# Kernel optimization log

Measured on AMD Instinct MI355X. Metric: run time of the kernel, lower is better.

## Reference

```python
import jax, jax.numpy as jnp
import numpy as np

B, S, D, H = 2, 2048, 1024, 16
DK = D // H


def setup_inputs() -> dict:
    key = jax.random.key(0)
    ks = jax.random.split(key, 12)
    scale = 1.0 / np.sqrt(D)
    inp = {
        "Q": jax.random.normal(ks[0], (B, S, D), jnp.float32),
        "K": jax.random.normal(ks[1], (B, S, D), jnp.float32),
        "V": jax.random.normal(ks[2], (B, S, D), jnp.float32),
        # causal mask, broadcastable to [B, H, S, S]; 0 -> masked
        "Mask": jnp.tril(jnp.ones((S, S), jnp.int32))[None, None],
        "Wq": jax.random.normal(ks[3], (D, D), jnp.float32) * scale,
        "bq": jnp.zeros((D,), jnp.float32),
        "Wk": jax.random.normal(ks[4], (D, D), jnp.float32) * scale,
        "bk": jnp.zeros((D,), jnp.float32),
        "Wv": jax.random.normal(ks[5], (D, D), jnp.float32) * scale,
        "bv": jnp.zeros((D,), jnp.float32),
        "Wo": jax.random.normal(ks[6], (D, D), jnp.float32) * scale,
        "bo": jnp.zeros((D,), jnp.float32),
    }
    return inp


def _heads(x):
    # [B, S, D] -> [B, H, S, DK]
    return x.reshape(B, S, H, DK).transpose(0, 2, 1, 3)


def reference(Q, K, V, Mask, Wq, bq, Wk, bk, Wv, bv, Wo, bo):
    q = _heads(Q @ Wq.T + bq)
    k = _heads(K @ Wk.T + bk)
    v = _heads(V @ Wv.T + bv)
    # NOTE: original module does NOT scale by 1/sqrt(d_k)
    logits = jnp.einsum("bhqd,bhkd->bhqk", q, k)
    logits = jnp.where(Mask == 0, jnp.float32(-1e9), logits)
    attn = jax.nn.softmax(logits, axis=-1)  # dropout p=0.0 -> identity
    ctx = jnp.einsum("bhqk,bhkd->bhqd", attn, v)
    ctx = ctx.transpose(0, 2, 1, 3).reshape(B, S, D)
    return ctx @ Wo.T + bo
```

## Files before the change

kernel.cpp:

```cpp
#include <hip/hip_runtime.h>
#include <hip/hip_bf16.h>

#define B_  2
#define S_  2048
#define D_  1024
#define H_  16
#define DK_ 64
#define M_  (B_ * S_)

typedef __bf16 bf16;
typedef __bf16 bf16x8 __attribute__((ext_vector_type(8)));
typedef __bf16 bf16x4 __attribute__((ext_vector_type(4)));
typedef float  f32x4  __attribute__((ext_vector_type(4)));

#define MFMA16(a, b, c) __builtin_amdgcn_mfma_f32_16x16x32_bf16((a), (b), (c), 0, 0, 0)

__device__ __forceinline__ void gl2lds16(const bf16* g, bf16* l) {
    __builtin_amdgcn_global_load_lds((const __attribute__((address_space(1))) void*)g,
                                     (__attribute__((address_space(3))) void*)l, 16, 0, 0);
}

struct CastArgs { const float* src[7]; bf16* dst[7]; };

__global__ __launch_bounds__(256) void cast_all(CastArgs a) {
    int i = blockIdx.x * 256 + threadIdx.x;
    int seg, off;
    if (i < 3145728) { seg = i >> 20; off = i & 1048575; }
    else { int j = i - 3145728; seg = 3 + (j >> 18); off = j & 262143; }
    float4 v = ((const float4*)a.src[seg])[off];
    bf16x4 o;
    o[0] = (bf16)v.x; o[1] = (bf16)v.y; o[2] = (bf16)v.z; o[3] = (bf16)v.w;
    *(bf16x4*)&a.dst[seg][(size_t)off * 4] = o;
}

struct QkvArgs { const bf16* A[3]; const bf16* W[3]; const float* bias[3]; bf16* out[3]; };

__global__ __launch_bounds__(256, 3) void gemm_qkv(QkvArgs ar) {
    __shared__ char smem[34816];
    bf16* As = (bf16*)smem;
    bf16* Bs = (bf16*)(smem + 16384);
    bf16* Cs = (bf16*)smem;

    const int z = blockIdx.z;
    const bf16* A  = ar.A[z];
    const bf16* Bt = ar.W[z];
    const float* bias = ar.bias[z];
    bf16* Out = ar.out[z];
    const int mode = (z == 2) ? 1 : 0;

    const int t = threadIdx.x, lane = t & 63, w = t >> 6;
    const int lr = lane & 15, lq = lane >> 4;
    const int wm = (w >> 1) * 64, wn = (w & 1) * 64;
    const int n0 = blockIdx.x * 128, m0 = blockIdx.y * 128;

    const bf16* Ag[4]; const bf16* Bg[4]; bf16* Al[4]; bf16* Bl[4];
#pragma unroll
    for (int i = 0; i < 4; ++i) {
        int c = i * 256 + w * 64 + lane;
        int row = c >> 3, x = (c & 7) ^ (row & 7);
        Ag[i] = A  + (size_t)(m0 + row) * 1024 + x * 8;
        Bg[i] = Bt + (size_t)(n0 + row) * 1024 + x * 8;
        Al[i] = As + (i * 256 + w * 64) * 8;
        Bl[i] = Bs + (i * 256 + w * 64) * 8;
    }

    f32x4 acc[4][4];
#pragma unroll
    for (int mi = 0; mi < 4; ++mi)
#pragma unroll
        for (int ni = 0; ni < 4; ++ni) acc[mi][ni] = 0.0f;

    for (int k0 = 0; k0 < 1024; k0 += 64) {
        __syncthreads();
#pragma unroll
        for (int i = 0; i < 4; ++i) {
            gl2lds16(Ag[i] + k0, Al[i]);
            gl2lds16(Bg[i] + k0, Bl[i]);
        }
        __syncthreads();
#pragma unroll
        for (int ks = 0; ks < 2; ++ks) {
            bf16x8 af[4], bfr[4];
#pragma unroll
            for (int mi = 0; mi < 4; ++mi) {
                int row = wm + mi * 16 + lr;
                af[mi] = *(const bf16x8*)&As[row * 64 + ((ks * 4 + lq) ^ (row & 7)) * 8];
            }
#pragma unroll
            for (int ni = 0; ni < 4; ++ni) {
                int row = wn + ni * 16 + lr;
                bfr[ni] = *(const bf16x8*)&Bs[row * 64 + ((ks * 4 + lq) ^ (row & 7)) * 8];
            }
#pragma unroll
            for (int mi = 0; mi < 4; ++mi)
#pragma unroll
                for (int ni = 0; ni < 4; ++ni) acc[mi][ni] = MFMA16(af[mi], bfr[ni], acc[mi][ni]);
        }
    }

    if (mode == 0) {
#pragma unroll
        for (int mi = 0; mi < 4; ++mi) {
#pragma unroll
            for (int ni = 0; ni < 4; ++ni) {
                int gn = n0 + wn + ni * 16 + lr;
                float bv = bias[gn];
#pragma unroll
                for (int r = 0; r < 4; ++r) {
                    int gm = m0 + wm + mi * 16 + lq * 4 + r;
                    float v = acc[mi][ni][r] + bv;
                    int b = gm >> 11, s = gm & (S_ - 1);
                    int h = gn >> 6, dk = gn & 63;
                    Out[(((size_t)(b * H_ + h) * S_ + s) << 6) + dk] = (bf16)v;
                }
            }
        }
    } else {
        __syncthreads();
#pragma unroll
        for (int mi = 0; mi < 4; ++mi) {
#pragma unroll
            for (int ni = 0; ni < 4; ++ni) {
                int n = wn + ni * 16 + lr;
                float bv = bias[n0 + n];
                bf16x4 pk;
#pragma unroll
                for (int r = 0; r < 4; ++r) pk[r] = (bf16)(acc[mi][ni][r] + bv);
                *(bf16x4*)&Cs[n * 136 + wm + mi * 16 + lq * 4] = pk;
            }
        }
        __syncthreads();
        const int b = m0 >> 11, s0 = m0 & (S_ - 1);
#pragma unroll
        for (int j = 0; j < 8; ++j) {
            int cc = j * 256 + t;
            int n = cc >> 4, cm = cc & 15;
            int gn = n0 + n, h = gn >> 6, dk = gn & 63;
            bf16x8 v = *(const bf16x8*)&Cs[n * 136 + cm * 8];
            *(bf16x8*)&Out[(((size_t)(b * H_ + h) * DK_ + dk) << 11) + s0 + cm * 8] = v;
        }
    }
}

__global__ __launch_bounds__(256, 2) void gemm_out(const bf16* __restrict__ A,
                                                   const bf16* __restrict__ Bt,
                                                   const float* __restrict__ bias,
                                                   float* __restrict__ Out) {
    __shared__ bf16 As[64 * 128];
    __shared__ bf16 Bs[128 * 128];

    const int t = threadIdx.x, lane = t & 63, w = t >> 6;
    const int lr = lane & 15, lq = lane >> 4;
    const int wm = (w >> 1) * 32, wn = (w & 1) * 64;
    const int n0 = blockIdx.x * 128, m0 = blockIdx.y * 64;

    const bf16* Ag[4]; bf16* Al[4];
#pragma unroll
    for (int i = 0; i < 4; ++i) {
        int c = i * 256 + w * 64 + lane;
        int row = c >> 4, x = (c & 15) ^ (row & 15);
        Ag[i] = A + (size_t)(m0 + row) * 1024 + x * 8;
        Al[i] = As + (i * 256 + w * 64) * 8;
    }
    const bf16* Bg[8]; bf16* Bl[8];
#pragma unroll
    for (int i = 0; i < 8; ++i) {
        int c = i * 256 + w * 64 + lane;
        int row = c >> 4, x = (c & 15) ^ (row & 15);
        Bg[i] = Bt + (size_t)(n0 + row) * 1024 + x * 8;
        Bl[i] = Bs + (i * 256 + w * 64) * 8;
    }

    f32x4 acc[2][4];
#pragma unroll
    for (int mi = 0; mi < 2; ++mi)
#pragma unroll
        for (int ni = 0; ni < 4; ++ni) acc[mi][ni] = 0.0f;

    for (int k0 = 0; k0 < 1024; k0 += 128) {
        __syncthreads();
#pragma unroll
        for (int i = 0; i < 4; ++i) gl2lds16(Ag[i] + k0, Al[i]);
#pragma unroll
        for (int i = 0; i < 8; ++i) gl2lds16(Bg[i] + k0, Bl[i]);
        __syncthreads();
#pragma unroll
        for (int ks = 0; ks < 4; ++ks) {
            bf16x8 af[2], bfr[4];
#pragma unroll
            for (int mi = 0; mi < 2; ++mi) {
                int row = wm + mi * 16 + lr;
                af[mi] = *(const bf16x8*)&As[row * 128 + (((ks * 4 + lq) ^ (row & 15))) * 8];
            }
#pragma unroll
            for (int ni = 0; ni < 4; ++ni) {
                int row = wn + ni * 16 + lr;
                bfr[ni] = *(const bf16x8*)&Bs[row * 128 + (((ks * 4 + lq) ^ (row & 15))) * 8];
            }
#pragma unroll
            for (int mi = 0; mi < 2; ++mi)
#pragma unroll
                for (int ni = 0; ni < 4; ++ni) acc[mi][ni] = MFMA16(af[mi], bfr[ni], acc[mi][ni]);
        }
    }

#pragma unroll
    for (int mi = 0; mi < 2; ++mi) {
#pragma unroll
        for (int ni = 0; ni < 4; ++ni) {
            int gn = n0 + wn + ni * 16 + lr;
            float bv = bias[gn];
#pragma unroll
            for (int r = 0; r < 4; ++r) {
                int gm = m0 + wm + mi * 16 + lq * 4 + r;
                Out[(size_t)gm * 1024 + gn] = acc[mi][ni][r] + bv;
            }
        }
    }
}

__global__ __launch_bounds__(256, 4) void flash_attn(const bf16* __restrict__ qh,
                                                     const bf16* __restrict__ kh,
                                                     const bf16* __restrict__ vt,
                                                     bf16* __restrict__ ctx) {
    __shared__ char smem[40960];
    bf16* Qs = (bf16*)smem;
    bf16* Ks = (bf16*)(smem + 8192);
    bf16* Ps = (bf16*)(smem + 24576);

    const int id = blockIdx.x;
    const int bh = (id & 7) * 4 + ((id >> 3) & 3);
    const int qt = id >> 5;
    const int b = bh >> 4, h = bh & 15;

    const bf16* Qp = qh + (size_t)bh * S_ * DK_;
    const bf16* Kp = kh + (size_t)bh * S_ * DK_;
    const bf16* Vp = vt + (size_t)bh * DK_ * S_;

    const int t = threadIdx.x, lane = t & 63, w = t >> 6;
    const int lr = lane & 15, lq = lane >> 4;
    const int wq = w & 1, wk = w >> 1;
    bf16* Pw = Ps + w * 2048;

#pragma unroll
    for (int i = 0; i < 2; ++i) {
        int c = w * 128 + i * 64 + lane;
        int qrow = c >> 3, xx = (c & 7) ^ (qrow & 7);
        gl2lds16(Qp + (size_t)(qt * 64 + qrow) * 64 + xx * 8, Qs + (w * 128 + i * 64) * 8);
    }

    f32x4 oacc[2][4];
#pragma unroll
    for (int mt = 0; mt < 2; ++mt)
#pragma unroll
        for (int nt = 0; nt < 4; ++nt) oacc[mt][nt] = 0.0f;
    float lpart[2] = {0.f, 0.f};

    const int nkt = qt / 2 + 1;
    for (int kt = 0; kt < nkt; ++kt) {
        __syncthreads();
#pragma unroll
        for (int i = 0; i < 4; ++i) {
            int c = w * 256 + i * 64 + lane;
            int krow = c >> 3, xx = (c & 7) ^ (krow & 7);
            gl2lds16(Kp + (size_t)(kt * 128 + krow) * 64 + xx * 8, Ks + (w * 256 + i * 64) * 8);
        }
        __syncthreads();

        const int k64 = kt * 2 + wk;
        if (k64 <= qt) {
            bf16x8 bv[2][4];
#pragma unroll
            for (int kk = 0; kk < 2; ++kk)
#pragma unroll
                for (int nt = 0; nt < 4; ++nt)
                    bv[kk][nt] = *(const bf16x8*)(Vp + (size_t)(nt * 16 + lr) * S_ +
                                                  kt * 128 + wk * 64 + kk * 32 + lq * 8);
            f32x4 s[4][2];
#pragma unroll
            for (int mt = 0; mt < 4; ++mt)
#pragma unroll
                for (int nt = 0; nt < 2; ++nt) s[mt][nt] = 0.0f;
#pragma unroll
            for (int ks = 0; ks < 2; ++ks) {
                bf16x8 af[4], qf[2];
                int xx = (ks * 4 + lq) ^ (lr & 7);
#pragma unroll
                for (int mt = 0; mt < 4; ++mt)
                    af[mt] = *(const bf16x8*)&Ks[(wk * 64 + mt * 16 + lr) * 64 + xx * 8];
#pragma unroll
                for (int nt = 0; nt < 2; ++nt)
                    qf[nt] = *(const bf16x8*)&Qs[(wq * 32 + nt * 16 + lr) * 64 + xx * 8];
#pragma unroll
                for (int mt = 0; mt < 4; ++mt)
#pragma unroll
                    for (int nt = 0; nt < 2; ++nt) s[mt][nt] = MFMA16(af[mt], qf[nt], s[mt][nt]);
            }
            const bool diag = (k64 == qt);
#pragma unroll
            for (int mt = 0; mt < 4; ++mt)
#pragma unroll
                for (int nt = 0; nt < 2; ++nt) {
                    bf16x4 pb;
#pragma unroll
                    for (int r = 0; r < 4; ++r) {
                        int kl = mt * 16 + lq * 4 + r;
                        int qlT = wq * 32 + nt * 16 + lr;
                        float p = (!diag || kl <= qlT) ? __expf(s[mt][nt][r]) : 0.0f;
                        bf16 p16 = (bf16)p;
                        lpart[nt] += (float)p16;
                        pb[r] = p16;
                    }
                    int xx = (2 * mt + (lq >> 1)) ^ (lr & 7);
                    *(bf16x4*)&Pw[(nt * 16 + lr) * 64 + xx * 8 + (lq & 1) * 4] = pb;
                }
#pragma unroll
            for (int kk = 0; kk < 2; ++kk) {
                bf16x8 ap[2];
                int xx = (kk * 4 + lq) ^ (lr & 7);
#pragma unroll
                for (int mt2 = 0; mt2 < 2; ++mt2)
                    ap[mt2] = *(const bf16x8*)&Pw[(mt2 * 16 + lr) * 64 + xx * 8];
#pragma unroll
                for (int mt2 = 0; mt2 < 2; ++mt2)
#pragma unroll
                    for (int nt = 0; nt < 4; ++nt)
                        oacc[mt2][nt] = MFMA16(ap[mt2], bv[kk][nt], oacc[mt2][nt]);
            }
        }
    }

    __syncthreads();
#pragma unroll
    for (int nt = 0; nt < 2; ++nt) {
        lpart[nt] += __shfl_xor(lpart[nt], 16);
        lpart[nt] += __shfl_xor(lpart[nt], 32);
    }
    float* Op = (float*)(smem + 24576);
    float* Lh = (float*)smem;
    if (lq == 0)
#pragma unroll
        for (int nt = 0; nt < 2; ++nt) Lh[wk * 64 + wq * 32 + nt * 16 + lr] = lpart[nt];
    if (wk == 1) {
#pragma unroll
        for (int mt = 0; mt < 2; ++mt)
#pragma unroll
            for (int nt = 0; nt < 4; ++nt)
#pragma unroll
                for (int r = 0; r < 4; ++r) {
                    int row = mt * 16 + lq * 4 + r, col = nt * 16 + lr;
                    int xx = (col >> 2) ^ (row & 15);
                    Op[wq * 2048 + row * 64 + xx * 4 + (col & 3)] = oacc[mt][nt][r];
                }
    }
    __syncthreads();
    if (wk == 0) {
        float linv[2][4];
#pragma unroll
        for (int mt = 0; mt < 2; ++mt)
#pragma unroll
            for (int r = 0; r < 4; ++r) {
                int qq = wq * 32 + mt * 16 + lq * 4 + r;
                linv[mt][r] = 1.0f / (Lh[qq] + Lh[64 + qq]);
            }
#pragma unroll
        for (int mt = 0; mt < 2; ++mt)
#pragma unroll
            for (int nt = 0; nt < 4; ++nt)
#pragma unroll
                for (int r = 0; r < 4; ++r) {
                    int row = mt * 16 + lq * 4 + r, col = nt * 16 + lr;
                    int xx = (col >> 2) ^ (row & 15);
                    float v = (oacc[mt][nt][r] + Op[wq * 2048 + row * 64 + xx * 4 + (col & 3)]) * linv[mt][r];
                    int q = qt * 64 + wq * 32 + row;
                    ctx[((size_t)(b * S_ + q)) * D_ + h * DK_ + col] = (bf16)v;
                }
    }
}

extern "C" void kernel_launch(void* const* d_in, const int* in_sizes, int n_in,
                              void* d_out, int out_size, void* d_ws, size_t ws_size,
                              hipStream_t stream) {
    const float* Q  = (const float*)d_in[0];
    const float* K  = (const float*)d_in[1];
    const float* V  = (const float*)d_in[2];
    const float* Wq = (const float*)d_in[4];
    const float* bq = (const float*)d_in[5];
    const float* Wk = (const float*)d_in[6];
    const float* bk = (const float*)d_in[7];
    const float* Wv = (const float*)d_in[8];
    const float* bv = (const float*)d_in[9];
    const float* Wo = (const float*)d_in[10];
    const float* bo = (const float*)d_in[11];

    char* p = (char*)d_ws;
    bf16* Qb  = (bf16*)p;  p += (size_t)M_ * D_ * 2;
    bf16* Kb  = (bf16*)p;  p += (size_t)M_ * D_ * 2;
    bf16* Vb  = (bf16*)p;  p += (size_t)M_ * D_ * 2;
    bf16* Wqb = (bf16*)p;  p += (size_t)D_ * D_ * 2;
    bf16* Wkb = (bf16*)p;  p += (size_t)D_ * D_ * 2;
    bf16* Wvb = (bf16*)p;  p += (size_t)D_ * D_ * 2;
    bf16* Wob = (bf16*)p;  p += (size_t)D_ * D_ * 2;
    bf16* qhd = (bf16*)p;  p += (size_t)M_ * D_ * 2;
    bf16* khd = (bf16*)p;  p += (size_t)M_ * D_ * 2;
    bf16* vtr = (bf16*)p;  p += (size_t)M_ * D_ * 2;
    bf16* ctx = (bf16*)p;  p += (size_t)M_ * D_ * 2;

    CastArgs ca;
    ca.src[0] = Q;  ca.dst[0] = Qb;
    ca.src[1] = K;  ca.dst[1] = Kb;
    ca.src[2] = V;  ca.dst[2] = Vb;
    ca.src[3] = Wq; ca.dst[3] = Wqb;
    ca.src[4] = Wk; ca.dst[4] = Wkb;
    ca.src[5] = Wv; ca.dst[5] = Wvb;
    ca.src[6] = Wo; ca.dst[6] = Wob;
    cast_all<<<16384, 256, 0, stream>>>(ca);

    QkvArgs qa;
    qa.A[0] = Qb;  qa.A[1] = Kb;  qa.A[2] = Vb;
    qa.W[0] = Wqb; qa.W[1] = Wkb; qa.W[2] = Wvb;
    qa.bias[0] = bq; qa.bias[1] = bk; qa.bias[2] = bv;
    qa.out[0] = qhd; qa.out[1] = khd; qa.out[2] = vtr;
    dim3 qgrid(D_ / 128, M_ / 128, 3);
    gemm_qkv<<<qgrid, 256, 0, stream>>>(qa);

    flash_attn<<<1024, 256, 0, stream>>>(qhd, khd, vtr, ctx);

    dim3 ogrid(D_ / 128, M_ / 64);
    gemm_out<<<ogrid, 256, 0, stream>>>(ctx, Wob, bo, (float*)d_out);
}
```

Before: 246.4 us.

## Stage GEMM epilogues through LDS for vector stores; reorder attention tiles

The QKV projection (mode 0) and output GEMM epilogues now write results to shared memory and then issue coalesced 16-byte vector stores, replacing scattered scalar stores. Shared memory in gemm_out grows to 51200 bytes to hold the fp32 staging tile, which may reduce occupancy. Flash attention now processes query tiles in reverse order so the longest causal tiles are scheduled first, and its launch bound drops from 4 to 3 blocks per CU. These changes aim to cut store inefficiency and tail imbalance, at the cost of extra syncs and LDS traffic.

Measured after the change: 231.2 us. -6.2%, faster.

```diff
diff --git a/kernel.cpp b/kernel.cpp
--- a/kernel.cpp
+++ b/kernel.cpp
@@ -98,25 +98,30 @@
         }
     }
 
+    __syncthreads();
     if (mode == 0) {
 #pragma unroll
         for (int mi = 0; mi < 4; ++mi) {
 #pragma unroll
             for (int ni = 0; ni < 4; ++ni) {
-                int gn = n0 + wn + ni * 16 + lr;
-                float bv = bias[gn];
-#pragma unroll
-                for (int r = 0; r < 4; ++r) {
-                    int gm = m0 + wm + mi * 16 + lq * 4 + r;
-                    float v = acc[mi][ni][r] + bv;
-                    int b = gm >> 11, s = gm & (S_ - 1);
-                    int h = gn >> 6, dk = gn & 63;
-                    Out[(((size_t)(b * H_ + h) * S_ + s) << 6) + dk] = (bf16)v;
-                }
-            }
+                int col = wn + ni * 16 + lr;
+                float bv = bias[n0 + col];
+#pragma unroll
+                for (int r = 0; r < 4; ++r)
+                    Cs[(wm + mi * 16 + lq * 4 + r) * 136 + col] = (bf16)(acc[mi][ni][r] + bv);
+            }
+        }
+        __syncthreads();
+#pragma unroll
+        for (int j = 0; j < 8; ++j) {
+            int cc = j * 256 + t;
+            int m = cc >> 4, cm = cc & 15;
+            int gm = m0 + m, b = gm >> 11, s = gm & (S_ - 1);
+            int gn = n0 + cm * 8, h = gn >> 6, dk = gn & 63;
+            *(bf16x8*)&Out[(((size_t)(b * H_ + h) * S_ + s) << 6) + dk] =
+                *(const bf16x8*)&Cs[m * 136 + cm * 8];
         }
     } else {
-        __syncthreads();
 #pragma unroll
         for (int mi = 0; mi < 4; ++mi) {
 #pragma unroll
@@ -146,8 +151,10 @@
                                                    const bf16* __restrict__ Bt,
                                                    const float* __restrict__ bias,
                                                    float* __restrict__ Out) {
-    __shared__ bf16 As[64 * 128];
-    __shared__ bf16 Bs[128 * 128];
+    __shared__ char smem[51200];
+    bf16* As = (bf16*)smem;
+    bf16* Bs = (bf16*)(smem + 16384);
+    float* Cs = (float*)(smem + 16384);
 
     const int t = threadIdx.x, lane = t & 63, w = t >> 6;
     const int lr = lane & 15, lq = lane >> 4;
@@ -204,22 +211,29 @@
         }
     }
 
+    __syncthreads();
 #pragma unroll
     for (int mi = 0; mi < 2; ++mi) {
 #pragma unroll
         for (int ni = 0; ni < 4; ++ni) {
-            int gn = n0 + wn + ni * 16 + lr;
-            float bv = bias[gn];
-#pragma unroll
-            for (int r = 0; r < 4; ++r) {
-                int gm = m0 + wm + mi * 16 + lq * 4 + r;
-                Out[(size_t)gm * 1024 + gn] = acc[mi][ni][r] + bv;
-            }
-        }
-    }
-}
-
-__global__ __launch_bounds__(256, 4) void flash_attn(const bf16* __restrict__ qh,
+            int col = wn + ni * 16 + lr;
+            float bv = bias[n0 + col];
+#pragma unroll
+            for (int r = 0; r < 4; ++r)
+                Cs[(wm + mi * 16 + lq * 4 + r) * 136 + col] = acc[mi][ni][r] + bv;
+        }
+    }
+    __syncthreads();
+#pragma unroll
+    for (int j = 0; j < 8; ++j) {
+        int cc = j * 256 + t;
+        int m = cc >> 5, cm = cc & 31;
+        *(f32x4*)&Out[(size_t)(m0 + m) * 1024 + n0 + cm * 4] =
+            *(const f32x4*)&Cs[m * 136 + cm * 4];
+    }
+}
+
+__global__ __launch_bounds__(256, 3) void flash_attn(const bf16* __restrict__ qh,
                                                      const bf16* __restrict__ kh,
                                                      const bf16* __restrict__ vt,
                                                      bf16* __restrict__ ctx) {
@@ -230,7 +244,7 @@
 
     const int id = blockIdx.x;
     const int bh = (id & 7) * 4 + ((id >> 3) & 3);
-    const int qt = id >> 5;
+    const int qt = 31 - (id >> 5);
     const int b = bh >> 4, h = bh & 15;
 
     const bf16* Qp = qh + (size_t)bh * S_ * DK_;
```
